# Kernel optimization log

Hardware: AMD Instinct MI355X
Metric: run time of the kernel (lower is better)

The kernel has to match this reference:

```python
import jax, jax.numpy as jnp
import numpy as np

ODE_UNFOLDS = 6   # ncps LTCCell default
EPS = 1e-8
BATCH = 4096

def _conv(x, w, b, stride, pad):
    y = jax.lax.conv_general_dilated(x, w, (stride, stride), [(pad, pad), (pad, pad)],
                                     dimension_numbers=('NCHW', 'OIHW', 'NCHW'))
    return y + b[None, :, None, None]

def _bn(x, g, bta, m, v):
    # eval-mode batchnorm (running stats)
    inv = g * jax.lax.rsqrt(v + 1e-5)
    return x * inv[None, :, None, None] + (bta - m * inv)[None, :, None, None]

def _maxpool2(x):
    return jax.lax.reduce_window(x, -jnp.inf, jax.lax.max, (1, 1, 2, 2), (1, 1, 2, 2), 'VALID')

def _forward(x, conv1_w, conv1_b, conv2_w, conv2_b, bn2_g, bn2_b, bn2_m, bn2_v,
             conv3_w, conv3_b, conv4_w, conv4_b, bn4_g, bn4_b, bn4_m, bn4_v,
             input_w, input_b, sensory_mu, sensory_sigma, sensory_w, sensory_erev, sensory_mask,
             mu, sigma, w, erev, mask, gleak, vleak, cm, output_w, output_b):
    h = jax.nn.relu(_conv(x, conv1_w, conv1_b, 1, 0))                                            # [B,16,26,26]
    h = jax.nn.relu(_bn(_conv(h, conv2_w, conv2_b, 2, 2), bn2_g, bn2_b, bn2_m, bn2_v))           # [B,32,14,14]
    h = jax.nn.relu(_conv(h, conv3_w, conv3_b, 2, 2))                                            # [B,64,7,7]
    h = _maxpool2(jax.nn.relu(_bn(_conv(h, conv4_w, conv4_b, 2, 2), bn4_g, bn4_b, bn4_m, bn4_v)))  # [B,128,2,2]
    seq = h.reshape(-1, 32, 16)                                                                  # [B,T=32,F=16]
    # --- LTC cell (ncps fused ODE solver) ---
    xin = seq * input_w + input_b                                                                # affine input mapping
    # sensory synapses depend only on the input -> precompute for all timesteps
    sact = jax.nn.softplus(sensory_w) * jax.nn.sigmoid((xin[..., None] - sensory_mu) * sensory_sigma) * sensory_mask  # [B,T,16,19]
    wnum_s = jnp.einsum('btsn,sn->btn', sact, sensory_erev)   # [B,T,19]
    wden_s = jnp.sum(sact, axis=2)                            # [B,T,19]
    w_pos = jax.nn.softplus(w) * mask                         # [pre=19,post=19]
    gl = jax.nn.softplus(gleak)
    cm_t = jax.nn.softplus(cm) * ODE_UNFOLDS                  # cm / (elapsed_time=1.0 / unfolds)
    def tstep(v, nd):
        wns, wds = nd
        def unfold(v2, _):
            wa = w_pos * jax.nn.sigmoid((v2[..., None] - mu) * sigma)   # [B,19,19]
            num = cm_t * v2 + gl * vleak + jnp.sum(wa * erev, axis=1) + wns
            den = cm_t + gl + jnp.sum(wa, axis=1) + wds
            return num / (den + EPS), None
        v, _ = jax.lax.scan(unfold, v, None, length=ODE_UNFOLDS)
        return v, None
    h0 = jnp.zeros((seq.shape[0], 19), seq.dtype)
    vT, _ = jax.lax.scan(tstep, h0, (jnp.swapaxes(wnum_s, 0, 1), jnp.swapaxes(wden_s, 0, 1)))
    # out[:, -1, :] == output mapping of final state; motor neurons are the first 2
    return vT[:, :2] * output_w + output_b


def setup_inputs() -> dict:
    key = jax.random.key(0)
    ks = jax.random.split(key, 16)
    rng = np.random.default_rng(0)
    u = lambda k, s, lo, hi: jax.random.uniform(k, s, jnp.float32, lo, hi)
    n = lambda k, s, sc: jax.random.normal(k, s, jnp.float32) * sc
    inp = {}
    inp['x'] = jax.random.normal(ks[0], (BATCH, 1, 28, 28), jnp.float32)
    inp['conv1_w'] = n(ks[1], (16, 1, 3, 3), 0.3); inp['conv1_b'] = jnp.zeros(16)
    inp['conv2_w'] = n(ks[2], (32, 16, 3, 3), 0.08); inp['conv2_b'] = jnp.zeros(32)
    inp['bn2_g'] = jnp.ones(32); inp['bn2_b'] = jnp.zeros(32)
    inp['bn2_m'] = jnp.zeros(32); inp['bn2_v'] = jnp.ones(32)
    inp['conv3_w'] = n(ks[3], (64, 32, 5, 5), 0.035); inp['conv3_b'] = jnp.zeros(64)
    inp['conv4_w'] = n(ks[4], (128, 64, 5, 5), 0.025); inp['conv4_b'] = jnp.zeros(128)
    inp['bn4_g'] = jnp.ones(128); inp['bn4_b'] = jnp.zeros(128)
    inp['bn4_m'] = jnp.zeros(128); inp['bn4_v'] = jnp.ones(128)
    inp['input_w'] = jnp.ones(16); inp['input_b'] = jnp.zeros(16)
    # ncps LTCCell init ranges
    inp['sensory_mu'] = u(ks[5], (16, 19), 0.3, 0.8)
    inp['sensory_sigma'] = u(ks[6], (16, 19), 3.0, 8.0)
    inp['sensory_w'] = u(ks[7], (16, 19), 0.001, 1.0)
    inp['sensory_erev'] = jnp.asarray(rng.choice([-1.0, 1.0], (16, 19)).astype(np.float32))
    inp['sensory_mask'] = jnp.asarray((rng.random((16, 19)) < 0.35).astype(np.float32))
    inp['mu'] = u(ks[8], (19, 19), 0.3, 0.8)
    inp['sigma'] = u(ks[9], (19, 19), 3.0, 8.0)
    inp['w'] = u(ks[10], (19, 19), 0.001, 1.0)
    inp['erev'] = jnp.asarray(rng.choice([-1.0, 1.0], (19, 19)).astype(np.float32))
    inp['mask'] = jnp.asarray((rng.random((19, 19)) < 0.35).astype(np.float32))
    inp['gleak'] = u(ks[11], (19,), 0.001, 1.0)
    inp['vleak'] = u(ks[12], (19,), -0.2, 0.2)
    inp['cm'] = u(ks[13], (19,), 0.4, 0.6)
    inp['output_w'] = jnp.ones(2); inp['output_b'] = jnp.zeros(2)
    return inp


def reference(x, conv1_w, conv1_b, conv2_w, conv2_b, bn2_g, bn2_b, bn2_m, bn2_v,
              conv3_w, conv3_b, conv4_w, conv4_b, bn4_g, bn4_b, bn4_m, bn4_v,
              input_w, input_b, sensory_mu, sensory_sigma, sensory_w, sensory_erev, sensory_mask,
              mu, sigma, w, erev, mask, gleak, vleak, cm, output_w, output_b):
    return _forward(x, conv1_w, conv1_b, conv2_w, conv2_b, bn2_g, bn2_b, bn2_m, bn2_v,
                    conv3_w, conv3_b, conv4_w, conv4_b, bn4_g, bn4_b, bn4_m, bn4_v,
                    input_w, input_b, sensory_mu, sensory_sigma, sensory_w, sensory_erev, sensory_mask,
                    mu, sigma, w, erev, mask, gleak, vleak, cm, output_w, output_b)
```

## Files before the change

### kernel.cpp

```cpp
#include <hip/hip_runtime.h>

#define BATCH 4096
typedef unsigned short u16_t;

#define P_SWM   0
#define P_SWME  304
#define P_WP    608
#define P_WPE   969
#define P_GL    1330
#define P_GLVL  1349
#define P_CMT   1368
#define P_SC2   1392
#define P_SH2   1424
#define P_SC4   1456
#define P_SH4   1584

#define OFF_PAR 0L
#define OFF_B2F 2048L
#define OFF_B3F 6656L
#define OFF_B4F 57856L
#define OFF_DYN 262656L

typedef __attribute__((ext_vector_type(8))) short short8;
typedef __attribute__((ext_vector_type(16))) float f32x16;
#define MFMA(a, b, c) __builtin_amdgcn_mfma_f32_32x32x16_bf16(a, b, c, 0, 0, 0)

#define PERM_HI(w1, w0) __builtin_amdgcn_perm((w1), (w0), 0x05040100u)
#define PERM_LO(w1, w0) __builtin_amdgcn_perm((w1), (w0), 0x07060302u)

union U8 { unsigned u[4]; short8 v; };

__device__ __forceinline__ float sigmoidf_(float x) {
    return 1.0f / (1.0f + __expf(-x));
}
__device__ __forceinline__ float softplusf_(float x) { return log1pf(__expf(x)); }

__device__ __forceinline__ unsigned splitpack(float f) {
    unsigned u = __float_as_uint(f);
    float rsd = f - __uint_as_float(u & 0xFFFF0000u);
    unsigned ur = __float_as_uint(rsd);
    ur = ur + 0x7FFFu + ((ur >> 16) & 1u);
    return (u >> 16) | (ur & 0xFFFF0000u);
}
__device__ __forceinline__ u16_t bfhalf(float v, int pl) {
    unsigned u = __float_as_uint(v);
    if (pl == 0) return (u16_t)(u >> 16);
    float rsd = v - __uint_as_float(u & 0xFFFF0000u);
    unsigned ur = __float_as_uint(rsd);
    ur = ur + 0x7FFFu + ((ur >> 16) & 1u);
    return (u16_t)(ur >> 16);
}

__global__ __launch_bounds__(256) void k_prep(
    const float* __restrict__ w2, const float* __restrict__ w3, const float* __restrict__ w4,
    const float* __restrict__ sw, const float* __restrict__ serev, const float* __restrict__ smask,
    const float* __restrict__ w,  const float* __restrict__ erev,  const float* __restrict__ mask,
    const float* __restrict__ gleak, const float* __restrict__ vleak, const float* __restrict__ cm,
    const float* __restrict__ b2, const float* __restrict__ g2, const float* __restrict__ be2,
    const float* __restrict__ m2, const float* __restrict__ v2,
    const float* __restrict__ b4, const float* __restrict__ g4, const float* __restrict__ be4,
    const float* __restrict__ m4, const float* __restrict__ v4,
    float* __restrict__ ws) {
    int gid = blockIdx.x * 256 + threadIdx.x, stride = gridDim.x * 256;
    u16_t* b2f = (u16_t*)(ws + OFF_B2F);
    u16_t* b3f = (u16_t*)(ws + OFF_B3F);
    u16_t* b4f = (u16_t*)(ws + OFF_B4F);
    for (int i = gid; i < 9216; i += stride) {
        int j = i & 7, ln = (i >> 3) & 63;
        int r = i >> 9;
        int s = r % 9, pl = r / 9;
        int k = s * 16 + (ln >> 5) * 8 + j;
        int tap = k >> 4, ci = k & 15;
        int co = ln & 31;
        b2f[i] = bfhalf(w2[(co * 16 + ci) * 9 + tap], pl);
    }
    for (int i = gid; i < 102400; i += stride) {
        int j = i & 7, ln = (i >> 3) & 63;
        int t = i >> 9;
        int s = t % 50, r = t / 50;
        int nt = r & 1, pl = r >> 1;
        int k = s * 16 + (ln >> 5) * 8 + j;
        int tap = k >> 5, ci = k & 31;
        int co = nt * 32 + (ln & 31);
        b3f[i] = bfhalf(w3[(co * 32 + ci) * 25 + tap], pl);
    }
    for (int i = gid; i < 409600; i += stride) {
        int j = i & 7, ln = (i >> 3) & 63;
        int t = i >> 9;
        int s = t % 100, r = t / 100;
        int nt = r & 3, pl = r >> 2;
        int k = s * 16 + (ln >> 5) * 8 + j;
        int tap = k >> 6, ci = k & 63;
        int co = nt * 32 + (ln & 31);
        b4f[i] = bfhalf(w4[(co * 64 + ci) * 25 + tap], pl);
    }
    if (blockIdx.x == 0) {
        float* par = ws + OFF_PAR;
        int tid = threadIdx.x;
        for (int i = tid; i < 304; i += 256) {
            float v_ = softplusf_(sw[i]) * smask[i];
            par[P_SWM + i] = v_;
            par[P_SWME + i] = v_ * serev[i];
        }
        for (int i = tid; i < 361; i += 256) {
            float v_ = softplusf_(w[i]) * mask[i];
            par[P_WP + i] = v_;
            par[P_WPE + i] = v_ * erev[i];
        }
        for (int i = tid; i < 19; i += 256) {
            float g = softplusf_(gleak[i]);
            par[P_GL + i] = g;
            par[P_GLVL + i] = g * vleak[i];
            par[P_CMT + i] = softplusf_(cm[i]) * 6.0f;
        }
        for (int i = tid; i < 32; i += 256) {
            float inv = g2[i] * __frsqrt_rn(v2[i] + 1e-5f);
            par[P_SC2 + i] = inv;
            par[P_SH2 + i] = (b2[i] - m2[i]) * inv + be2[i];
        }
        for (int i = tid; i < 128; i += 256) {
            float inv = g4[i] * __frsqrt_rn(v4[i] + 1e-5f);
            par[P_SC4 + i] = inv;
            par[P_SH4 + i] = (b4[i] - m4[i]) * inv + be4[i];
        }
    }
}

__global__ __launch_bounds__(256, 2) void k_conv12(
    const float* __restrict__ x, const float* __restrict__ w1, const float* __restrict__ b1,
    const float* __restrict__ ws, unsigned* __restrict__ h2g) {
    __shared__ float xs[784];
    __shared__ unsigned h1s[14300];
    const float* par = ws + OFF_PAR;
    int b = blockIdx.x, tid = threadIdx.x;
    {
        for (int i = tid; i < 784; i += 256) xs[i] = x[(long)b * 784 + i];
        uint4* hz = (uint4*)h1s;
        uint4 z; z.x = z.y = z.z = z.w = 0u;
        for (int i = tid; i < 3575; i += 256) hz[i] = z;
    }
    __syncthreads();
    {
        int co = tid >> 4, slot = tid & 15;
        float wr[9];
        #pragma unroll
        for (int i = 0; i < 9; i++) wr[i] = w1[co * 9 + i];
        float bb = b1[co];
        for (int k = 0; k < 43; k++) {
            int px = slot + (k << 4);
            if (px >= 676) break;
            int oh = px / 26, ow = px % 26;
            float s = bb;
            #pragma unroll
            for (int kh = 0; kh < 3; kh++)
                #pragma unroll
                for (int kw = 0; kw < 3; kw++)
                    s = fmaf(xs[(oh + kh) * 28 + ow + kw], wr[kh * 3 + kw], s);
            h1s[((oh + 2) * 29 + (ow + 2)) * 17 + co] = splitpack(fmaxf(s, 0.f));
        }
    }
    __syncthreads();
    {
        int wv = tid >> 6, lane = tid & 63;
        int mloc = lane & 31, hf = lane >> 5, half8 = hf * 8;
        const u16_t* B2 = (const u16_t*)(ws + OFF_B2F);
        const short8* pb = (const short8*)B2 + lane;
        float sc = par[P_SC2 + mloc], sh = par[P_SH2 + mloc];
        for (int tix = 0; tix < 2; tix++) {
            int mt = wv + tix * 4;
            if (mt >= 7) break;
            int px = mt * 32 + mloc;
            bool pxok = px < 196;
            int pxc = pxok ? px : 195;
            int oh = pxc / 14, ow = pxc % 14;
            f32x16 acc;
            #pragma unroll
            for (int i = 0; i < 16; i++) acc[i] = 0.f;
            #pragma unroll
            for (int s = 0; s < 9; s++) {
                int kh = s / 3, kw = s % 3;
                int abase = (pxok ? ((oh * 2 + kh) * 29 + (ow * 2 + kw)) * 17 : 0) + half8;
                unsigned w_[8];
                #pragma unroll
                for (int j = 0; j < 8; j++) w_[j] = h1s[abase + j];
                U8 ah, al;
                #pragma unroll
                for (int d = 0; d < 4; d++) {
                    ah.u[d] = PERM_HI(w_[2 * d + 1], w_[2 * d]);
                    al.u[d] = PERM_LO(w_[2 * d + 1], w_[2 * d]);
                }
                short8 bh = pb[s * 64];
                short8 bl = pb[(9 + s) * 64];
                acc = MFMA(ah.v, bh, acc);
                acc = MFMA(ah.v, bl, acc);
                acc = MFMA(al.v, bh, acc);
            }
            #pragma unroll
            for (int r5 = 0; r5 < 16; r5++) {
                int row = (r5 & 3) + 8 * (r5 >> 2) + 4 * hf;
                int pxw = mt * 32 + row;
                if (pxw < 196) {
                    float y = fmaxf(fmaf(acc[r5], sc, sh), 0.f);
                    h2g[(long)b * 6272 + pxw * 32 + mloc] = splitpack(y);
                }
            }
        }
    }
}

__global__ __launch_bounds__(256, 4) void k_conv34s(
    const unsigned* __restrict__ h2g, const float* __restrict__ b3g,
    const float* __restrict__ inw, const float* __restrict__ inb,
    const float* __restrict__ smu, const float* __restrict__ ssig,
    const float* __restrict__ ws,
    float* __restrict__ wn, float* __restrict__ wd) {
    __shared__ unsigned h2s[6698];
    __shared__ unsigned h3s[3300];
    const float* par = ws + OFF_PAR;
    int b = blockIdx.x, tid = threadIdx.x;
    {
        const unsigned* src = h2g + (long)b * 6272;
        for (int i = tid; i < 6272; i += 256) {
            int px = i >> 5, ci = i & 31;
            h2s[px * 34 + ci] = src[i];
        }
        if (tid < 34) h2s[196 * 34 + tid] = 0u;
        if (tid < 66) h3s[49 * 66 + tid] = 0u;
    }
    __syncthreads();
    int wv = tid >> 6;
    int lane = tid & 63;
    int mloc = lane & 31, hf = lane >> 5, half8 = hf * 8;

    {
        int mt = wv & 1, nt = wv >> 1;
        int px = mt * 32 + mloc;
        int oh = px / 7, ow = px % 7;
        bool pxok = px < 49;
        int oh2 = oh * 2 - 2, ow2 = ow * 2 - 2;
        int co3 = nt * 32 + mloc;
        float bias = b3g[co3];
        f32x16 acc;
        #pragma unroll
        for (int i = 0; i < 16; i++) acc[i] = bias;
        const u16_t* B3 = (const u16_t*)(ws + OFF_B3F);
        const short8* pbh = (const short8*)(B3 + (long)(nt * 50) * 512) + lane;
        const short8* pbl = (const short8*)(B3 + (long)((2 + nt) * 50) * 512) + lane;
        int s = 0;
        for (int kh = 0; kh < 5; kh++) {
            int ih = oh2 + kh;
            #pragma unroll
            for (int kw = 0; kw < 5; kw++) {
                int iw = ow2 + kw;
                bool ok = pxok && ((unsigned)ih < 14u) && ((unsigned)iw < 14u);
                int rowb = (ok ? (ih * 14 + iw) : 196) * 34;
                #pragma unroll
                for (int sub = 0; sub < 2; sub++) {
                    const uint2* ap = (const uint2*)(h2s + rowb + sub * 16 + half8);
                    uint2 p0 = ap[0], p1 = ap[1], p2 = ap[2], p3 = ap[3];
                    U8 ah, al;
                    ah.u[0] = PERM_HI(p0.y, p0.x); al.u[0] = PERM_LO(p0.y, p0.x);
                    ah.u[1] = PERM_HI(p1.y, p1.x); al.u[1] = PERM_LO(p1.y, p1.x);
                    ah.u[2] = PERM_HI(p2.y, p2.x); al.u[2] = PERM_LO(p2.y, p2.x);
                    ah.u[3] = PERM_HI(p3.y, p3.x); al.u[3] = PERM_LO(p3.y, p3.x);
                    short8 bh = pbh[s * 64];
                    short8 bl = pbl[s * 64];
                    acc = MFMA(ah.v, bh, acc);
                    acc = MFMA(ah.v, bl, acc);
                    acc = MFMA(al.v, bh, acc);
                    s++;
                }
            }
        }
        #pragma unroll
        for (int r5 = 0; r5 < 16; r5++) {
            int row = (r5 & 3) + 8 * (r5 >> 2) + 4 * hf;
            int pxw = mt * 32 + row;
            if (pxw < 49) {
                float y = fmaxf(acc[r5], 0.f);
                h3s[pxw * 66 + co3] = splitpack(y);
            }
        }
    }
    __syncthreads();
    {
        int oh = mloc >> 2, ow = mloc & 3;
        bool pxok = mloc < 16;
        int oh2 = oh * 2 - 2, ow2 = ow * 2 - 2;
        int co4 = wv * 32 + mloc;
        f32x16 acc;
        #pragma unroll
        for (int i = 0; i < 16; i++) acc[i] = 0.f;
        const u16_t* B4 = (const u16_t*)(ws + OFF_B4F);
        const short8* pbh = (const short8*)(B4 + (long)(wv * 100) * 512) + lane;
        const short8* pbl = (const short8*)(B4 + (long)((4 + wv) * 100) * 512) + lane;
        int s = 0;
        for (int kh = 0; kh < 5; kh++) {
            int ih = oh2 + kh;
            #pragma unroll
            for (int kw = 0; kw < 5; kw++) {
                int iw = ow2 + kw;
                bool ok = pxok && ((unsigned)ih < 7u) && ((unsigned)iw < 7u);
                int rowb = (ok ? (ih * 7 + iw) : 49) * 66;
                #pragma unroll
                for (int sub = 0; sub < 4; sub++) {
                    const uint2* ap = (const uint2*)(h3s + rowb + sub * 16 + half8);
                    uint2 p0 = ap[0], p1 = ap[1], p2 = ap[2], p3 = ap[3];
                    U8 ah, al;
                    ah.u[0] = PERM_HI(p0.y, p0.x); al.u[0] = PERM_LO(p0.y, p0.x);
                    ah.u[1] = PERM_HI(p1.y, p1.x); al.u[1] = PERM_LO(p1.y, p1.x);
                    ah.u[2] = PERM_HI(p2.y, p2.x); al.u[2] = PERM_LO(p2.y, p2.x);
                    ah.u[3] = PERM_HI(p3.y, p3.x); al.u[3] = PERM_LO(p3.y, p3.x);
                    short8 bh = pbh[s * 64];
                    short8 bl = pbl[s * 64];
                    acc = MFMA(ah.v, bh, acc);
                    acc = MFMA(ah.v, bl, acc);
                    acc = MFMA(al.v, bh, acc);
                    s++;
                }
            }
        }
        float sc = par[P_SC4 + co4], sh = par[P_SH4 + co4];
        float y[8];
        #pragma unroll
        for (int p = 0; p < 8; p++) y[p] = fmaxf(fmaf(acc[p], sc, sh), 0.f);
        __syncthreads();
        float* xin_s = (float*)h2s;
        #pragma unroll
        for (int q = 0; q < 4; q++) {
            int ph = q >> 1, pw = q & 1;
            int r1 = ph * 4 + pw * 2;
            float part = fmaxf(y[r1], y[r1 + 1]);
            part = fmaxf(part, __shfl_xor(part, 32));
            if (lane < 32) {
                int f = ((co4 & 3) << 2) + q;
                xin_s[(co4 >> 2) * 16 + f] = fmaf(part, inw[f], inb[f]);
            }
        }
    }
    __syncthreads();
    const float* xin_s = (const float*)h2s;
    for (int idx = tid; idx < 608; idx += 256) {
        int tt = idx / 19, n = idx - tt * 19;
        float nu = 0.f, de = 0.f;
        #pragma unroll
        for (int s = 0; s < 16; s++) {
            float sg = sigmoidf_((xin_s[tt * 16 + s] - smu[s * 19 + n]) * ssig[s * 19 + n]);
            nu = fmaf(par[P_SWME + s * 19 + n], sg, nu);
            de = fmaf(par[P_SWM + s * 19 + n], sg, de);
        }
        wn[((long)b * 32 + tt) * 19 + n] = nu;
        wd[((long)b * 32 + tt) * 19 + n] = de;
    }
}

__global__ __launch_bounds__(256, 2) void k_ltc(
    const float* __restrict__ mu_g, const float* __restrict__ sg_g,
    const float* __restrict__ ws,
    const float* __restrict__ wn, const float* __restrict__ wd,
    const float* __restrict__ outw, const float* __restrict__ outb,
    float* __restrict__ out, int img0, int nimg) {
    const float* par = ws + OFF_PAR;
    int tid = threadIdx.x, wave = tid >> 6, lane = tid & 63;
    int li = lane / 19, j = lane - li * 19;
    if (li > 2) { li = 2; j = 18; }
    int il = blockIdx.x * 12 + wave * 3 + li;
    int ilc = il < nimg ? il : nimg - 1;

    const float L2E = 1.44269504f;
    float aj[19], bj[19], wpj[19], wpej[19];
    #pragma unroll
    for (int i = 0; i < 19; i++) {
        float mu = mu_g[i * 19 + j];
        float sg = sg_g[i * 19 + j];
        aj[i] = -sg * L2E;
        bj[i] = mu * sg * L2E;
        wpj[i] = par[P_WP + i * 19 + j];
        wpej[i] = par[P_WPE + i * 19 + j];
    }
    float cmt = par[P_CMT + j], gl = par[P_GL + j], glvl = par[P_GLVL + j];
    float v = 0.f;
    long base0 = (long)ilc * 608 + j;
    float wns = wn[base0], wds = wd[base0];
    for (int t = 0; t < 32; t++) {
        float wns_n = 0.f, wds_n = 0.f;
        if (t < 31) {
            long basen = base0 + (t + 1) * 19;
            wns_n = wn[basen];
            wds_n = wd[basen];
        }
        #pragma unroll 1
        for (int u = 0; u < 6; u++) {
            float n0 = 0.f, n1 = 0.f, d0 = 0.f, d1 = 0.f;
            #pragma unroll
            for (int i = 0; i < 19; i++) {
                float vi = __shfl(v, li * 19 + i, 64);
                float e = __builtin_amdgcn_exp2f(fmaf(vi, aj[i], bj[i]));
                float s = __builtin_amdgcn_rcpf(1.0f + e);
                if (i & 1) { n1 = fmaf(wpej[i], s, n1); d1 = fmaf(wpj[i], s, d1); }
                else       { n0 = fmaf(wpej[i], s, n0); d0 = fmaf(wpj[i], s, d0); }
            }
            float num = fmaf(cmt, v, glvl) + wns + (n0 + n1);
            float den = cmt + gl + wds + (d0 + d1);
            v = num * __builtin_amdgcn_rcpf(den + 1e-8f);
        }
        wns = wns_n; wds = wds_n;
    }
    if (j < 2 && il < nimg && lane < 57)
        out[(long)(img0 + il) * 2 + j] = fmaf(v, outw[j], outb[j]);
}

extern "C" void kernel_launch(void* const* d_in, const int* in_sizes, int n_in,
                              void* d_out, int out_size, void* d_ws, size_t ws_size,
                              hipStream_t stream) {
    const float* x    = (const float*)d_in[0];
    const float* w1   = (const float*)d_in[1];
    const float* b1   = (const float*)d_in[2];
    const float* w2   = (const float*)d_in[3];
    const float* b2   = (const float*)d_in[4];
    const float* g2   = (const float*)d_in[5];
    const float* be2  = (const float*)d_in[6];
    const float* m2   = (const float*)d_in[7];
    const float* v2   = (const float*)d_in[8];
    const float* w3   = (const float*)d_in[9];
    const float* b3   = (const float*)d_in[10];
    const float* w4   = (const float*)d_in[11];
    const float* b4   = (const float*)d_in[12];
    const float* g4   = (const float*)d_in[13];
    const float* be4  = (const float*)d_in[14];
    const float* m4   = (const float*)d_in[15];
    const float* v4   = (const float*)d_in[16];
    const float* inw  = (const float*)d_in[17];
    const float* inb  = (const float*)d_in[18];
    const float* smu  = (const float*)d_in[19];
    const float* ssig = (const float*)d_in[20];
    const float* sw   = (const float*)d_in[21];
    const float* serv = (const float*)d_in[22];
    const float* smk  = (const float*)d_in[23];
    const float* mu_  = (const float*)d_in[24];
    const float* sig_ = (const float*)d_in[25];
    const float* w_   = (const float*)d_in[26];
    const float* erev = (const float*)d_in[27];
    const float* mask = (const float*)d_in[28];
    const float* glk  = (const float*)d_in[29];
    const float* vlk  = (const float*)d_in[30];
    const float* cm   = (const float*)d_in[31];
    const float* outw = (const float*)d_in[32];
    const float* outb = (const float*)d_in[33];
    float* ws = (float*)d_ws;

    k_prep<<<64, 256, 0, stream>>>(w2, w3, w4, sw, serv, smk, w_, erev, mask,
                                   glk, vlk, cm, b2, g2, be2, m2, v2,
                                   b4, g4, be4, m4, v4, ws);

    long avail = (long)(ws_size / 4) - OFF_DYN;
    long per = 6272 + 1216;
    int chunk = (int)(avail / per);
    if (chunk > BATCH) chunk = BATCH;
    if (chunk < 1) chunk = 1;

    float* wnp = ws + OFF_DYN;
    float* wdp = wnp + (long)chunk * 608;
    unsigned* h2 = (unsigned*)(wdp + (long)chunk * 608);

    for (int c0 = 0; c0 < BATCH; c0 += chunk) {
        int n = (BATCH - c0 < chunk) ? (BATCH - c0) : chunk;
        k_conv12<<<n, 256, 0, stream>>>(x + (long)c0 * 784, w1, b1, ws, h2);
        k_conv34s<<<n, 256, 0, stream>>>(h2, b3, inw, inb, smu, ssig, ws, wnp, wdp);
        k_ltc<<<(n + 11) / 12, 256, 0, stream>>>(mu_, sig_, ws, wnp, wdp, outw, outb,
                                                 (float*)d_out, c0, n);
    }
}
```

Before: 604.3 us.

## Widen conv blocks to 512 threads and process two images per conv34 block

k_conv12 moves to 512 threads so each wave handles a single conv2 M-tile, and the conv1 loop runs over twice as many slots. k_conv34s now packs two images into one 512-thread block with doubled shared buffers, and pads rows to an odd stride (33/65) instead of 34/66, presumably to cut LDS bank conflicts. That padding forces the vectorized uint2 loads to become scalar loads. The aim is more waves in flight per block and fewer blocks, at the cost of larger LDS use per block, which may cap occupancy.

Measured after the change: 602.8 us. About the same (-0.2%).

```diff
diff --git a/kernel.cpp b/kernel.cpp
--- a/kernel.cpp
+++ b/kernel.cpp
@@ -126,7 +126,7 @@
     }
 }
 
-__global__ __launch_bounds__(256, 2) void k_conv12(
+__global__ __launch_bounds__(512, 4) void k_conv12(
     const float* __restrict__ x, const float* __restrict__ w1, const float* __restrict__ b1,
     const float* __restrict__ ws, unsigned* __restrict__ h2g) {
     __shared__ float xs[784];
@@ -134,20 +134,20 @@
     const float* par = ws + OFF_PAR;
     int b = blockIdx.x, tid = threadIdx.x;
     {
-        for (int i = tid; i < 784; i += 256) xs[i] = x[(long)b * 784 + i];
+        for (int i = tid; i < 784; i += 512) xs[i] = x[(long)b * 784 + i];
         uint4* hz = (uint4*)h1s;
         uint4 z; z.x = z.y = z.z = z.w = 0u;
-        for (int i = tid; i < 3575; i += 256) hz[i] = z;
+        for (int i = tid; i < 3575; i += 512) hz[i] = z;
     }
     __syncthreads();
     {
-        int co = tid >> 4, slot = tid & 15;
+        int co = tid >> 5, slot = tid & 31;
         float wr[9];
         #pragma unroll
         for (int i = 0; i < 9; i++) wr[i] = w1[co * 9 + i];
         float bb = b1[co];
-        for (int k = 0; k < 43; k++) {
-            int px = slot + (k << 4);
+        for (int k = 0; k < 22; k++) {
+            int px = slot + (k << 5);
             if (px >= 676) break;
             int oh = px / 26, ow = px % 26;
             float s = bb;
@@ -166,9 +166,8 @@
         const u16_t* B2 = (const u16_t*)(ws + OFF_B2F);
         const short8* pb = (const short8*)B2 + lane;
         float sc = par[P_SC2 + mloc], sh = par[P_SH2 + mloc];
-        for (int tix = 0; tix < 2; tix++) {
-            int mt = wv + tix * 4;
-            if (mt >= 7) break;
+        int mt = wv;
+        if (mt < 7) {
             int px = mt * 32 + mloc;
             bool pxok = px < 196;
             int pxc = pxok ? px : 195;
@@ -208,24 +207,33 @@
     }
 }
 
-__global__ __launch_bounds__(256, 4) void k_conv34s(
+__global__ __launch_bounds__(512, 4) void k_conv34s(
     const unsigned* __restrict__ h2g, const float* __restrict__ b3g,
     const float* __restrict__ inw, const float* __restrict__ inb,
     const float* __restrict__ smu, const float* __restrict__ ssig,
     const float* __restrict__ ws,
-    float* __restrict__ wn, float* __restrict__ wd) {
-    __shared__ unsigned h2s[6698];
-    __shared__ unsigned h3s[3300];
+    float* __restrict__ wn, float* __restrict__ wd, int nimg) {
+    __shared__ unsigned h2s[13002];
+    __shared__ unsigned h3s[6500];
     const float* par = ws + OFF_PAR;
     int b = blockIdx.x, tid = threadIdx.x;
-    {
-        const unsigned* src = h2g + (long)b * 6272;
-        for (int i = tid; i < 6272; i += 256) {
-            int px = i >> 5, ci = i & 31;
-            h2s[px * 34 + ci] = src[i];
-        }
-        if (tid < 34) h2s[196 * 34 + tid] = 0u;
-        if (tid < 66) h3s[49 * 66 + tid] = 0u;
+    int g0 = b * 2;
+    int g1 = (g0 + 1 < nimg) ? g0 + 1 : g0;
+    {
+        const unsigned* s0 = h2g + (long)g0 * 6272;
+        const unsigned* s1 = h2g + (long)g1 * 6272;
+        for (int i = tid; i < 12544; i += 512) {
+            int img = i >> 12 >> 1;
+            img = i / 6272;
+            int r = i - img * 6272;
+            int px = r >> 5, ci = r & 31;
+            h2s[img * 6501 + px * 33 + ci] = (img ? s1 : s0)[r];
+        }
+        if (tid < 66) h2s[(tid >> 5 >> 0 < 1 ? 0 : 0)] = h2s[0];
+        if (tid < 33) h2s[196 * 33 + tid] = 0u;
+        else if (tid < 66) h2s[6501 + 196 * 33 + (tid - 33)] = 0u;
+        if (tid < 65) h3s[49 * 65 + tid] = 0u;
+        else if (tid < 130) h3s[3250 + 49 * 65 + (tid - 65)] = 0u;
     }
     __syncthreads();
     int wv = tid >> 6;
@@ -233,7 +241,8 @@
     int mloc = lane & 31, hf = lane >> 5, half8 = hf * 8;
 
     {
-        int mt = wv & 1, nt = wv >> 1;
+        int img = wv >> 2, mt = wv & 1, nt = (wv >> 1) & 1;
+        int imgo2 = img * 6501;
         int px = mt * 32 + mloc;
         int oh = px / 7, ow = px % 7;
         bool pxok = px < 49;
@@ -253,16 +262,19 @@
             for (int kw = 0; kw < 5; kw++) {
                 int iw = ow2 + kw;
                 bool ok = pxok && ((unsigned)ih < 14u) && ((unsigned)iw < 14u);
-                int rowb = (ok ? (ih * 14 + iw) : 196) * 34;
+                int rowb = imgo2 + (ok ? (ih * 14 + iw) : 196) * 33;
                 #pragma unroll
                 for (int sub = 0; sub < 2; sub++) {
-                    const uint2* ap = (const uint2*)(h2s + rowb + sub * 16 + half8);
-                    uint2 p0 = ap[0], p1 = ap[1], p2 = ap[2], p3 = ap[3];
+                    const unsigned* ap = h2s + rowb + sub * 16 + half8;
+                    unsigned w_[8];
+                    #pragma unroll
+                    for (int j = 0; j < 8; j++) w_[j] = ap[j];
                     U8 ah, al;
-                    ah.u[0] = PERM_HI(p0.y, p0.x); al.u[0] = PERM_LO(p0.y, p0.x);
-                    ah.u[1] = PERM_HI(p1.y, p1.x); al.u[1] = PERM_LO(p1.y, p1.x);
-                    ah.u[2] = PERM_HI(p2.y, p2.x); al.u[2] = PERM_LO(p2.y, p2.x);
-                    ah.u[3] = PERM_HI(p3.y, p3.x); al.u[3] = PERM_LO(p3.y, p3.x);
+                    #pragma unroll
+                    for (int d = 0; d < 4; d++) {
+                        ah.u[d] = PERM_HI(w_[2 * d + 1], w_[2 * d]);
+                        al.u[d] = PERM_LO(w_[2 * d + 1], w_[2 * d]);
+                    }
                     short8 bh = pbh[s * 64];
                     short8 bl = pbl[s * 64];
                     acc = MFMA(ah.v, bh, acc);
@@ -278,22 +290,24 @@
             int pxw = mt * 32 + row;
             if (pxw < 49) {
                 float y = fmaxf(acc[r5], 0.f);
-                h3s[pxw * 66 + co3] = splitpack(y);
+                h3s[img * 3250 + pxw * 65 + co3] = splitpack(y);
             }
         }
     }
     __syncthreads();
     {
+        int img = wv >> 2, nt = wv & 3;
+        int imgo3 = img * 3250;
         int oh = mloc >> 2, ow = mloc & 3;
         bool pxok = mloc < 16;
         int oh2 = oh * 2 - 2, ow2 = ow * 2 - 2;
-        int co4 = wv * 32 + mloc;
+        int co4 = nt * 32 + mloc;
         f32x16 acc;
         #pragma unroll
         for (int i = 0; i < 16; i++) acc[i] = 0.f;
         const u16_t* B4 = (const u16_t*)(ws + OFF_B4F);
-        const short8* pbh = (const short8*)(B4 + (long)(wv * 100) * 512) + lane;
-        const short8* pbl = (const short8*)(B4 + (long)((4 + wv) * 100) * 512) + lane;
+        const short8* pbh = (const short8*)(B4 + (long)(nt * 100) * 512) + lane;
+        const short8* pbl = (const short8*)(B4 + (long)((4 + nt) * 100) * 512) + lane;
         int s = 0;
         for (int kh = 0; kh < 5; kh++) {
             int ih = oh2 + kh;
@@ -301,16 +315,19 @@
             for (int kw = 0; kw < 5; kw++) {
                 int iw = ow2 + kw;
                 bool ok = pxok && ((unsigned)ih < 7u) && ((unsigned)iw < 7u);
-                int rowb = (ok ? (ih * 7 + iw) : 49) * 66;
+                int rowb = imgo3 + (ok ? (ih * 7 + iw) : 49) * 65;
                 #pragma unroll
                 for (int sub = 0; sub < 4; sub++) {
-                    const uint2* ap = (const uint2*)(h3s + rowb + sub * 16 + half8);
-                    uint2 p0 = ap[0], p1 = ap[1], p2 = ap[2], p3 = ap[3];
+                    const unsigned* ap = h3s + rowb + sub * 16 + half8;
+                    unsigned w_[8];
+                    #pragma unroll
+                    for (int j = 0; j < 8; j++) w_[j] = ap[j];
                     U8 ah, al;
-                    ah.u[0] = PERM_HI(p0.y, p0.x); al.u[0] = PERM_LO(p0.y, p0.x);
-                    ah.u[1] = PERM_HI(p1.y, p1.x); al.u[1] = PERM_LO(p1.y, p1.x);
-                    ah.u[2] = PERM_HI(p2.y, p2.x); al.u[2] = PERM_LO(p2.y, p2.x);
-                    ah.u[3] = PERM_HI(p3.y, p3.x); al.u[3] = PERM_LO(p3.y, p3.x);
+                    #pragma unroll
+                    for (int d = 0; d < 4; d++) {
+                        ah.u[d] = PERM_HI(w_[2 * d + 1], w_[2 * d]);
+                        al.u[d] = PERM_LO(w_[2 * d + 1], w_[2 * d]);
+                    }
                     short8 bh = pbh[s * 64];
                     short8 bl = pbl[s * 64];
                     acc = MFMA(ah.v, bh, acc);
@@ -334,23 +351,27 @@
             part = fmaxf(part, __shfl_xor(part, 32));
             if (lane < 32) {
                 int f = ((co4 & 3) << 2) + q;
-                xin_s[(co4 >> 2) * 16 + f] = fmaf(part, inw[f], inb[f]);
+                xin_s[img * 512 + (co4 >> 2) * 16 + f] = fmaf(part, inw[f], inb[f]);
             }
         }
     }
     __syncthreads();
     const float* xin_s = (const float*)h2s;
-    for (int idx = tid; idx < 608; idx += 256) {
-        int tt = idx / 19, n = idx - tt * 19;
+    for (int idx = tid; idx < 1216; idx += 512) {
+        int img = idx / 608;
+        int r = idx - img * 608;
+        int tt = r / 19, n = r - tt * 19;
+        int gi = g0 + img;
+        if (gi >= nimg) break;
         float nu = 0.f, de = 0.f;
         #pragma unroll
         for (int s = 0; s < 16; s++) {
-            float sg = sigmoidf_((xin_s[tt * 16 + s] - smu[s * 19 + n]) * ssig[s * 19 + n]);
+            float sg = sigmoidf_((xin_s[img * 512 + tt * 16 + s] - smu[s * 19 + n]) * ssig[s * 19 + n]);
             nu = fmaf(par[P_SWME + s * 19 + n], sg, nu);
             de = fmaf(par[P_SWM + s * 19 + n], sg, de);
         }
-        wn[((long)b * 32 + tt) * 19 + n] = nu;
-        wd[((long)b * 32 + tt) * 19 + n] = de;
+        wn[((long)gi * 32 + tt) * 19 + n] = nu;
+        wd[((long)gi * 32 + tt) * 19 + n] = de;
     }
 }
 
@@ -457,7 +478,8 @@
     long per = 6272 + 1216;
     int chunk = (int)(avail / per);
     if (chunk > BATCH) chunk = BATCH;
-    if (chunk < 1) chunk = 1;
+    if (chunk < 2) chunk = 2;
+    if (chunk > BATCH) chunk = BATCH;
 
     float* wnp = ws + OFF_DYN;
     float* wdp = wnp + (long)chunk * 608;
@@ -465,8 +487,9 @@
 
     for (int c0 = 0; c0 < BATCH; c0 += chunk) {
         int n = (BATCH - c0 < chunk) ? (BATCH - c0) : chunk;
-        k_conv12<<<n, 256, 0, stream>>>(x + (long)c0 * 784, w1, b1, ws, h2);
-        k_conv34s<<<n, 256, 0, stream>>>(h2, b3, inw, inb, smu, ssig, ws, wnp, wdp);
+        k_conv12<<<n, 512, 0, stream>>>(x + (long)c0 * 784, w1, b1, ws, h2);
+        k_conv34s<<<(n + 1) / 2, 512, 0, stream>>>(h2, b3, inw, inb, smu, ssig, ws,
+                                                   wnp, wdp, n);
         k_ltc<<<(n + 11) / 12, 256, 0, stream>>>(mu_, sig_, ws, wnp, wdp, outw, outb,
                                                  (float*)d_out, c0, n);
     }
```
